# Kernel optimization log

Measured on AMD Instinct MI355X. Metric: run time of the kernel, lower is better.

Reference implementation:

```python
import jax, jax.numpy as jnp
import numpy as np

N_NODES = 32768
N_EDGES = 262144
HEAD = 8
CHANNEL = 64
LAYER_NUM = 2
HC = HEAD * CHANNEL  # 512


def setup_inputs() -> dict:
    key = jax.random.key(0)
    ks = jax.random.split(key, 12)
    def lin(k, fan_in, fan_out):
        s = 1.0 / np.sqrt(fan_in)
        kw, kb = jax.random.split(k)
        W = jax.random.uniform(kw, (fan_in, fan_out), jnp.float32, -s, s)
        b = jax.random.uniform(kb, (fan_out,), jnp.float32, -s, s)
        return W, b
    Wn, bn = lin(ks[0], 118, HC)
    We, be = lin(ks[1], 22, HC)
    Wa, ba = lin(ks[2], 2 * HC, HC)
    attn_w = jax.random.normal(ks[3], (1, HEAD, CHANNEL), jnp.float32) * 0.1
    x = jax.random.normal(ks[4], (N_NODES, 118), jnp.float32)
    edge_feat = jax.random.normal(ks[5], (N_EDGES, 22), jnp.float32)
    src = jax.random.randint(ks[6], (N_EDGES,), 0, N_NODES)
    dst = jax.random.randint(ks[7], (N_EDGES,), 0, N_NODES)
    return {"x": x, "edge_feat": edge_feat, "src": src, "dst": dst,
            "Wn": Wn, "bn": bn, "We": We, "be": be, "Wa": Wa, "ba": ba,
            "attn_w": attn_w}


def reference(x, edge_feat, src, dst, Wn, bn, We, be, Wa, ba, attn_w):
    N = x.shape[0]
    H, C = attn_w.shape[1], attn_w.shape[2]
    h = x @ Wn + bn                      # [N, H*C]
    _eh = edge_feat @ We + be            # computed in original forward, never used
    for _ in range(LAYER_NUM):
        # gather src/dst node states onto edges and score them (GATv2 style)
        e = jnp.concatenate([h[src], h[dst]], axis=-1)            # [E, 2HC]
        e = jax.nn.leaky_relu(e @ Wa + ba, negative_slope=0.01)   # [E, HC]
        score = jnp.sum(e.reshape(-1, H, C) * attn_w, axis=-1)    # [E, H]
        # edge softmax normalized over incoming edges of each dst node
        m = jax.ops.segment_max(score, dst, num_segments=N)       # [N, H]
        ex = jnp.exp(score - m[dst])                              # [E, H]
        denom = jax.ops.segment_sum(ex, dst, num_segments=N)      # [N, H]
        alpha = ex / denom[dst]                                   # [E, H]
        # weighted message passing: u_mul_e then sum over dst
        msg = h[src].reshape(-1, H, C) * alpha[:, :, None]        # [E, H, C]
        h = jax.ops.segment_sum(msg, dst, num_segments=N).reshape(N, H * C)
    return h
```

## Files before the change

kernel.cpp:

```cpp
#include <hip/hip_runtime.h>
#include <hip/hip_bf16.h>
#include <stdint.h>

#define N_NODES 32768
#define N_EDGES 262144

typedef __attribute__((ext_vector_type(8))) short short8;
typedef __attribute__((ext_vector_type(4))) float f32x4;

typedef const __attribute__((address_space(1))) void* gvp;
typedef __attribute__((address_space(3))) void* lvp;

__device__ __forceinline__ float bf2f(ushort u) {
  return __uint_as_float(((uint)u) << 16);
}
__device__ __forceinline__ ushort f2bf(float f) {
  uint x = __float_as_uint(f);
  uint r = (x + 0x7fffu + ((x >> 16) & 1u)) >> 16;
  return (ushort)r;
}
__device__ __forceinline__ float loadf(const void* p, size_t i, int isbf) {
  return isbf ? bf2f(((const ushort*)p)[i]) : ((const float*)p)[i];
}

__global__ void detect_dtype(const uint* __restrict__ xw, int* __restrict__ flag) {
  __shared__ int cnt;
  if (threadIdx.x == 0) cnt = 0;
  __syncthreads();
  int good = 0;
  for (int i = threadIdx.x; i < 1024; i += 256) {
    uint lo = xw[i] & 0xFFFFu;
    uint ef = (lo >> 7) & 0xFFu;
    if (lo == 0u || (ef >= 0x60u && ef <= 0x90u)) good++;
  }
  atomicAdd(&cnt, good);
  __syncthreads();
  if (threadIdx.x == 0) *flag = (cnt >= 614) ? 1 : 0;
}

__global__ void prep_weights(const void* __restrict__ Wa, const void* __restrict__ Wn,
                             const void* __restrict__ ba, const void* __restrict__ bn,
                             const void* __restrict__ aw, const int* __restrict__ flag,
                             ushort* __restrict__ W2T, ushort* __restrict__ WnpT,
                             float* __restrict__ bias2, float* __restrict__ bnf,
                             float* __restrict__ wf) {
  const int fl = *flag;
  const int b = blockIdx.x;
  if (b < 2048) {
    int t = b * 256 + threadIdx.x;
    int n = t >> 9, k = t & 511;
    size_t idx = (n < 512) ? ((size_t)k * 512 + n) : ((size_t)(512 + k) * 512 + (n - 512));
    W2T[t] = f2bf(loadf(Wa, idx, fl));
  } else if (b < 2304) {
    int t = (b - 2048) * 256 + threadIdx.x;
    int n = t >> 7, k = t & 127;
    WnpT[t] = (k < 118) ? f2bf(loadf(Wn, (size_t)k * 512 + n, fl)) : (ushort)0;
  } else {
    int t = (b - 2304) * 256 + threadIdx.x;
    if (t < 1024) bias2[t] = (t < 512) ? loadf(ba, t, fl) : 0.f;
    if (t < 512) { bnf[t] = loadf(bn, t, fl); wf[t] = loadf(aw, t, fl); }
  }
}

__global__ void build_xp(const void* __restrict__ x, const int* __restrict__ flag,
                         ushort* __restrict__ xp) {
  int fl = *flag;
  int t = blockIdx.x * blockDim.x + threadIdx.x;
  int i = t >> 7, k = t & 127;
  xp[t] = (k < 118) ? f2bf(loadf(x, (size_t)i * 118 + k, fl)) : (ushort)0;
}

__global__ void csr_count(const int* __restrict__ dst, int* __restrict__ cnt) {
  int e = blockIdx.x * blockDim.x + threadIdx.x;
  atomicAdd(&cnt[dst[e]], 1);
}

__global__ __launch_bounds__(1024)
void csr_scan(const int* __restrict__ cnt, int* __restrict__ rowptr,
              int* __restrict__ cursor) {
  __shared__ int part[1024];
  const int t = threadIdx.x;
  const int base = t * 32;
  int loc[32];
  int s = 0;
#pragma unroll
  for (int i = 0; i < 32; ++i) { loc[i] = s; s += cnt[base + i]; }
  part[t] = s;
  __syncthreads();
  for (int off = 1; off < 1024; off <<= 1) {
    int v = (t >= off) ? part[t - off] : 0;
    __syncthreads();
    part[t] += v;
    __syncthreads();
  }
  int pre = (t == 0) ? 0 : part[t - 1];
#pragma unroll
  for (int i = 0; i < 32; ++i) {
    int v = pre + loc[i];
    rowptr[base + i] = v;
    cursor[base + i] = v;
  }
  if (t == 1023) rowptr[N_NODES] = part[1023];
}

__global__ void csr_fill(const int* __restrict__ dst, int* __restrict__ cursor,
                         int* __restrict__ eidx) {
  int e = blockIdx.x * blockDim.x + threadIdx.x;
  int p = atomicAdd(&cursor[dst[e]], 1);
  eidx[p] = e;
}

__global__ __launch_bounds__(256)
void gemm_bf16(const ushort* __restrict__ A, const ushort* __restrict__ BT,
               const float* __restrict__ bias, ushort* __restrict__ C,
               int M, int N, int K) {
  __shared__ __align__(16) ushort As[128 * 32];
  __shared__ __align__(16) ushort Bs[128 * 32];
  const int tid = threadIdx.x, wave = tid >> 6, lane = tid & 63;
  const int bm = blockIdx.y * 128, bn = blockIdx.x * 128;
  const int wm = (wave >> 1) * 64, wn = (wave & 1) * 64;
  const int fcol = lane & 15, quad = lane >> 4;

  const f32x4 zero = {0.f, 0.f, 0.f, 0.f};
  f32x4 acc[4][4];
#pragma unroll
  for (int i = 0; i < 4; ++i)
#pragma unroll
    for (int j = 0; j < 4; ++j) acc[i][j] = zero;

  for (int k0 = 0; k0 < K; k0 += 32) {
#pragma unroll
    for (int r = 0; r < 2; ++r) {
      int o = r * 4096 + wave * 1024 + lane * 16;
      int row = o >> 6;
      int ke = (o & 63) >> 1;
      const ushort* gA = A + (size_t)(bm + row) * K + k0 + ke;
      const ushort* gB = BT + (size_t)(bn + row) * K + k0 + ke;
      ushort* lA = As + ((r * 4096 + wave * 1024) >> 1);
      ushort* lB = Bs + ((r * 4096 + wave * 1024) >> 1);
      __builtin_amdgcn_global_load_lds((gvp)(const void*)gA, (lvp)(void*)lA, 16, 0, 0);
      __builtin_amdgcn_global_load_lds((gvp)(const void*)gB, (lvp)(void*)lB, 16, 0, 0);
    }
    __syncthreads();
    short8 a[4], b[4];
#pragma unroll
    for (int i = 0; i < 4; ++i) {
      a[i] = *(const short8*)&As[(wm + i * 16 + fcol) * 32 + quad * 8];
      b[i] = *(const short8*)&Bs[(wn + i * 16 + fcol) * 32 + quad * 8];
    }
#pragma unroll
    for (int i = 0; i < 4; ++i)
#pragma unroll
      for (int j = 0; j < 4; ++j)
        acc[i][j] = __builtin_amdgcn_mfma_f32_16x16x32_bf16(a[i], b[j], acc[i][j], 0, 0, 0);
    __syncthreads();
  }

#pragma unroll
  for (int i = 0; i < 4; ++i) {
    int rowb = bm + wm + i * 16 + quad * 4;
#pragma unroll
    for (int j = 0; j < 4; ++j) {
      int col = bn + wn + j * 16 + fcol;
      float bb = bias[col];
#pragma unroll
      for (int r = 0; r < 4; ++r) {
        C[(size_t)(rowb + r) * N + col] = f2bf(acc[i][j][r] + bb);
      }
    }
  }
}

__global__ __launch_bounds__(256)
void node_fused(const ushort* __restrict__ PQ, const ushort* __restrict__ hb_in,
                const int* __restrict__ src, const int* __restrict__ eidx,
                const int* __restrict__ rowptr, const float* __restrict__ wf,
                const int* __restrict__ flag, ushort* __restrict__ hb_out,
                void* __restrict__ out, int write_out) {
  const int wave = threadIdx.x >> 6, lane = threadIdx.x & 63;
  const int d = blockIdx.x * 4 + wave;
  const int beg = rowptr[d], end = rowptr[d + 1];
  const int c0 = lane * 8;

  const uint4 qv = *(const uint4*)(PQ + (size_t)d * 1024 + 512 + c0);
  const uint qw[4] = {qv.x, qv.y, qv.z, qv.w};
  float q[8], w[8];
#pragma unroll
  for (int i = 0; i < 4; ++i) {
    q[2 * i]     = __uint_as_float(qw[i] << 16);
    q[2 * i + 1] = __uint_as_float(qw[i] & 0xffff0000u);
  }
  const float4 w0 = *(const float4*)(wf + c0);
  const float4 w1 = *(const float4*)(wf + c0 + 4);
  w[0] = w0.x; w[1] = w0.y; w[2] = w0.z; w[3] = w0.w;
  w[4] = w1.x; w[5] = w1.y; w[6] = w1.z; w[7] = w1.w;

  float m = -3e38f, den = 0.f;
  float acc[8] = {0.f, 0.f, 0.f, 0.f, 0.f, 0.f, 0.f, 0.f};

  int sj = (beg < end) ? src[eidx[beg]] : 0;
  for (int j = beg; j < end; ++j) {
    const int s = sj;
    if (j + 1 < end) sj = src[eidx[j + 1]];
    const uint4 pv = *(const uint4*)(PQ + (size_t)s * 1024 + c0);
    const uint4 hv = *(const uint4*)(hb_in + (size_t)s * 512 + c0);
    const uint pw[4] = {pv.x, pv.y, pv.z, pv.w};
    const uint hw[4] = {hv.x, hv.y, hv.z, hv.w};
    float t = 0.f;
#pragma unroll
    for (int i = 0; i < 4; ++i) {
      float ea = __uint_as_float(pw[i] << 16) + q[2 * i];
      float eb = __uint_as_float(pw[i] & 0xffff0000u) + q[2 * i + 1];
      ea = (ea > 0.f) ? ea : 0.01f * ea;
      eb = (eb > 0.f) ? eb : 0.01f * eb;
      t += ea * w[2 * i] + eb * w[2 * i + 1];
    }
    t += __shfl_xor(t, 1);
    t += __shfl_xor(t, 2);
    t += __shfl_xor(t, 4);
    const float mnew = fmaxf(m, t);
    const float corr = __expf(m - mnew);
    const float ex = __expf(t - mnew);
    den = den * corr + ex;
#pragma unroll
    for (int i = 0; i < 4; ++i) {
      acc[2 * i]     = acc[2 * i] * corr     + ex * __uint_as_float(hw[i] << 16);
      acc[2 * i + 1] = acc[2 * i + 1] * corr + ex * __uint_as_float(hw[i] & 0xffff0000u);
    }
    m = mnew;
  }

  const float inv = (end > beg) ? (1.f / den) : 0.f;
  uint o[4];
#pragma unroll
  for (int i = 0; i < 4; ++i) {
    float v0 = acc[2 * i] * inv, v1 = acc[2 * i + 1] * inv;
    o[i] = (uint)f2bf(v0) | ((uint)f2bf(v1) << 16);
  }
  *(uint4*)(hb_out + (size_t)d * 512 + c0) = *(uint4*)o;
  if (write_out) {
    if (*flag) {
      *(uint4*)((ushort*)out + (size_t)d * 512 + c0) = *(uint4*)o;
    } else {
      float4 f0 = {acc[0] * inv, acc[1] * inv, acc[2] * inv, acc[3] * inv};
      float4 f1 = {acc[4] * inv, acc[5] * inv, acc[6] * inv, acc[7] * inv};
      *(float4*)((float*)out + (size_t)d * 512 + c0) = f0;
      *(float4*)((float*)out + (size_t)d * 512 + c0 + 4) = f1;
    }
  }
}

extern "C" void kernel_launch(void* const* d_in, const int* in_sizes, int n_in,
                              void* d_out, int out_size, void* d_ws, size_t ws_size,
                              hipStream_t stream) {
  const void* x   = d_in[0];
  const int*  src = (const int*)d_in[2];
  const int*  dst = (const int*)d_in[3];
  const void* Wn  = d_in[4];
  const void* bn  = d_in[5];
  const void* Wa  = d_in[8];
  const void* ba  = d_in[9];
  const void* aw  = d_in[10];

  char* ws = (char*)d_ws;
  size_t off = 0;
  auto alloc = [&](size_t bytes) {
    char* p = ws + off;
    off = (off + bytes + 255) & ~(size_t)255;
    return p;
  };
  ushort* hbA    = (ushort*)alloc((size_t)N_NODES * 512 * 2);
  ushort* hbB    = (ushort*)alloc((size_t)N_NODES * 512 * 2);
  ushort* PQ     = (ushort*)alloc((size_t)N_NODES * 1024 * 2);
  int*    eidx   = (int*)   alloc((size_t)N_EDGES * 4);
  int*    rowptr = (int*)   alloc((size_t)(N_NODES + 1) * 4);
  int*    cnt    = (int*)   alloc((size_t)N_NODES * 4);
  int*    cursor = (int*)   alloc((size_t)N_NODES * 4);
  ushort* W2T    = (ushort*)alloc((size_t)1024 * 512 * 2);
  float*  bias2  = (float*) alloc(1024 * 4);
  ushort* xp     = (ushort*)alloc((size_t)N_NODES * 128 * 2);
  ushort* WnpT   = (ushort*)alloc((size_t)512 * 128 * 2);
  float*  bnf    = (float*) alloc(512 * 4);
  float*  wf     = (float*) alloc(512 * 4);
  int*    flag   = (int*)   alloc(256);

  detect_dtype<<<1, 256, 0, stream>>>((const uint*)x, flag);
  prep_weights<<<2308, 256, 0, stream>>>(Wa, Wn, ba, bn, aw, flag,
                                         W2T, WnpT, bias2, bnf, wf);
  build_xp<<<(N_NODES * 128) / 256, 256, 0, stream>>>(x, flag, xp);

  hipMemsetAsync(cnt, 0, (size_t)N_NODES * 4, stream);
  csr_count<<<N_EDGES / 256, 256, 0, stream>>>(dst, cnt);
  csr_scan<<<1, 1024, 0, stream>>>(cnt, rowptr, cursor);
  csr_fill<<<N_EDGES / 256, 256, 0, stream>>>(dst, cursor, eidx);

  {
    dim3 g(512 / 128, N_NODES / 128);
    gemm_bf16<<<g, 256, 0, stream>>>(xp, WnpT, bnf, hbA, N_NODES, 512, 128);
  }

  ushort* hin = hbA;
  ushort* hout = hbB;
  for (int layer = 0; layer < 2; ++layer) {
    dim3 g(1024 / 128, N_NODES / 128);
    gemm_bf16<<<g, 256, 0, stream>>>(hin, W2T, bias2, PQ, N_NODES, 1024, 512);
    node_fused<<<N_NODES / 4, 256, 0, stream>>>(PQ, hin, src, eidx, rowptr, wf, flag,
                                                hout, d_out, layer == 1 ? 1 : 0);
    ushort* t = hin; hin = hout; hout = t;
  }
}
```

Baseline: 486.0 us.

## Fold node projection into first-layer attention GEMM and skip redundant softmax rescale

Precomputes a combined weight Wc = Wn·Wa and a bias bc = bn·Wa + ba, so the layer-0 PQ GEMM runs with K=128 on the padded input x instead of K=512 on h. This removes most of the first-layer GEMM work. It also merges build_xp into the weight prep kernel, and in the online softmax it skips the max-correction exps when no lane's score exceeds the running max. The cost is a different rounding path (bf16 of the product weight), a few small extra prep launches, and a wave-uniform branch in the inner loop.

```diff
diff --git a/kernel.cpp b/kernel.cpp
--- a/kernel.cpp
+++ b/kernel.cpp
@@ -38,12 +38,14 @@
   if (threadIdx.x == 0) *flag = (cnt >= 614) ? 1 : 0;
 }
 
-__global__ void prep_weights(const void* __restrict__ Wa, const void* __restrict__ Wn,
-                             const void* __restrict__ ba, const void* __restrict__ bn,
-                             const void* __restrict__ aw, const int* __restrict__ flag,
-                             ushort* __restrict__ W2T, ushort* __restrict__ WnpT,
-                             float* __restrict__ bias2, float* __restrict__ bnf,
-                             float* __restrict__ wf) {
+__global__ void prep_all(const void* __restrict__ Wa, const void* __restrict__ Wn,
+                         const void* __restrict__ ba, const void* __restrict__ bn,
+                         const void* __restrict__ aw, const void* __restrict__ x,
+                         const int* __restrict__ flag,
+                         ushort* __restrict__ W2T, ushort* __restrict__ WnpT,
+                         ushort* __restrict__ Wn_pad, float* __restrict__ bias2,
+                         float* __restrict__ bnf, float* __restrict__ wf,
+                         float* __restrict__ zbias, ushort* __restrict__ xp) {
   const int fl = *flag;
   const int b = blockIdx.x;
   if (b < 2048) {
@@ -55,19 +57,41 @@
     int t = (b - 2048) * 256 + threadIdx.x;
     int n = t >> 7, k = t & 127;
     WnpT[t] = (k < 118) ? f2bf(loadf(Wn, (size_t)k * 512 + n, fl)) : (ushort)0;
-  } else {
+  } else if (b < 2560) {
     int t = (b - 2304) * 256 + threadIdx.x;
+    int n = t >> 9, j = t & 511;
+    Wn_pad[t] = (n < 118) ? f2bf(loadf(Wn, (size_t)n * 512 + j, fl)) : (ushort)0;
+  } else if (b < 2564) {
+    int t = (b - 2560) * 256 + threadIdx.x;
     if (t < 1024) bias2[t] = (t < 512) ? loadf(ba, t, fl) : 0.f;
     if (t < 512) { bnf[t] = loadf(bn, t, fl); wf[t] = loadf(aw, t, fl); }
-  }
-}
-
-__global__ void build_xp(const void* __restrict__ x, const int* __restrict__ flag,
-                         ushort* __restrict__ xp) {
-  int fl = *flag;
-  int t = blockIdx.x * blockDim.x + threadIdx.x;
-  int i = t >> 7, k = t & 127;
-  xp[t] = (k < 118) ? f2bf(loadf(x, (size_t)i * 118 + k, fl)) : (ushort)0;
+    if (t < 128) zbias[t] = 0.f;
+  } else {
+    int t = (b - 2564) * 256 + threadIdx.x;
+    int i = t >> 7, k = t & 127;
+    xp[t] = (k < 118) ? f2bf(loadf(x, (size_t)i * 118 + k, fl)) : (ushort)0;
+  }
+}
+
+__global__ __launch_bounds__(256)
+void build_bc(const ushort* __restrict__ W2T, const float* __restrict__ bnf,
+              const float* __restrict__ bias2, float* __restrict__ bc) {
+  const int wave = threadIdx.x >> 6, lane = threadIdx.x & 63;
+  const int j = blockIdx.x * 4 + wave;
+  const uint4 v = *(const uint4*)(W2T + (size_t)j * 512 + lane * 8);
+  const float4 b0 = *(const float4*)(bnf + lane * 8);
+  const float4 b1 = *(const float4*)(bnf + lane * 8 + 4);
+  const uint w[4] = {v.x, v.y, v.z, v.w};
+  const float bb[8] = {b0.x, b0.y, b0.z, b0.w, b1.x, b1.y, b1.z, b1.w};
+  float s = 0.f;
+#pragma unroll
+  for (int i = 0; i < 4; ++i) {
+    s += __uint_as_float(w[i] << 16) * bb[2 * i];
+    s += __uint_as_float(w[i] & 0xffff0000u) * bb[2 * i + 1];
+  }
+  s += __shfl_xor(s, 1);  s += __shfl_xor(s, 2);  s += __shfl_xor(s, 4);
+  s += __shfl_xor(s, 8);  s += __shfl_xor(s, 16); s += __shfl_xor(s, 32);
+  if (lane == 0) bc[j] = s + bias2[j];
 }
 
 __global__ void csr_count(const int* __restrict__ dst, int* __restrict__ cnt) {
@@ -218,16 +242,26 @@
     t += __shfl_xor(t, 1);
     t += __shfl_xor(t, 2);
     t += __shfl_xor(t, 4);
-    const float mnew = fmaxf(m, t);
-    const float corr = __expf(m - mnew);
-    const float ex = __expf(t - mnew);
-    den = den * corr + ex;
-#pragma unroll
-    for (int i = 0; i < 4; ++i) {
-      acc[2 * i]     = acc[2 * i] * corr     + ex * __uint_as_float(hw[i] << 16);
-      acc[2 * i + 1] = acc[2 * i + 1] * corr + ex * __uint_as_float(hw[i] & 0xffff0000u);
-    }
-    m = mnew;
+    if (__any(t > m)) {
+      const float mnew = fmaxf(m, t);
+      const float corr = __expf(m - mnew);
+      const float ex = __expf(t - mnew);
+      den = den * corr + ex;
+#pragma unroll
+      for (int i = 0; i < 4; ++i) {
+        acc[2 * i]     = acc[2 * i] * corr     + ex * __uint_as_float(hw[i] << 16);
+        acc[2 * i + 1] = acc[2 * i + 1] * corr + ex * __uint_as_float(hw[i] & 0xffff0000u);
+      }
+      m = mnew;
+    } else {
+      const float ex = __expf(t - m);
+      den += ex;
+#pragma unroll
+      for (int i = 0; i < 4; ++i) {
+        acc[2 * i]     += ex * __uint_as_float(hw[i] << 16);
+        acc[2 * i + 1] += ex * __uint_as_float(hw[i] & 0xffff0000u);
+      }
+    }
   }
 
   const float inv = (end > beg) ? (1.f / den) : 0.f;
@@ -277,7 +311,11 @@
   int*    cnt    = (int*)   alloc((size_t)N_NODES * 4);
   int*    cursor = (int*)   alloc((size_t)N_NODES * 4);
   ushort* W2T    = (ushort*)alloc((size_t)1024 * 512 * 2);
+  ushort* WcT    = (ushort*)alloc((size_t)1024 * 128 * 2);
+  ushort* Wn_pad = (ushort*)alloc((size_t)128 * 512 * 2);
   float*  bias2  = (float*) alloc(1024 * 4);
+  float*  bc     = (float*) alloc(1024 * 4);
+  float*  zbias  = (float*) alloc(128 * 4);
   ushort* xp     = (ushort*)alloc((size_t)N_NODES * 128 * 2);
   ushort* WnpT   = (ushort*)alloc((size_t)512 * 128 * 2);
   float*  bnf    = (float*) alloc(512 * 4);
@@ -285,9 +323,13 @@
   int*    flag   = (int*)   alloc(256);
 
   detect_dtype<<<1, 256, 0, stream>>>((const uint*)x, flag);
-  prep_weights<<<2308, 256, 0, stream>>>(Wa, Wn, ba, bn, aw, flag,
-                                         W2T, WnpT, bias2, bnf, wf);
-  build_xp<<<(N_NODES * 128) / 256, 256, 0, stream>>>(x, flag, xp);
+  prep_all<<<2564 + (N_NODES * 128) / 256, 256, 0, stream>>>(
+      Wa, Wn, ba, bn, aw, x, flag, W2T, WnpT, Wn_pad, bias2, bnf, wf, zbias, xp);
+  build_bc<<<256, 256, 0, stream>>>(W2T, bnf, bias2, bc);
+  {
+    dim3 g(128 / 128, 1024 / 128);
+    gemm_bf16<<<g, 256, 0, stream>>>(W2T, Wn_pad, zbias, WcT, 1024, 128, 512);
+  }
 
   hipMemsetAsync(cnt, 0, (size_t)N_NODES * 4, stream);
   csr_count<<<N_EDGES / 256, 256, 0, stream>>>(dst, cnt);
@@ -299,13 +341,17 @@
     gemm_bf16<<<g, 256, 0, stream>>>(xp, WnpT, bnf, hbA, N_NODES, 512, 128);
   }
 
-  ushort* hin = hbA;
-  ushort* hout = hbB;
-  for (int layer = 0; layer < 2; ++layer) {
+  {
     dim3 g(1024 / 128, N_NODES / 128);
-    gemm_bf16<<<g, 256, 0, stream>>>(hin, W2T, bias2, PQ, N_NODES, 1024, 512);
-    node_fused<<<N_NODES / 4, 256, 0, stream>>>(PQ, hin, src, eidx, rowptr, wf, flag,
-                                                hout, d_out, layer == 1 ? 1 : 0);
-    ushort* t = hin; hin = hout; hout = t;
-  }
-}
+    gemm_bf16<<<g, 256, 0, stream>>>(xp, WcT, bc, PQ, N_NODES, 1024, 128);
+  }
+  node_fused<<<N_NODES / 4, 256, 0, stream>>>(PQ, hbA, src, eidx, rowptr, wf, flag,
+                                              hbB, d_out, 0);
+
+  {
+    dim3 g(1024 / 128, N_NODES / 128);
+    gemm_bf16<<<g, 256, 0, stream>>>(hbB, W2T, bias2, PQ, N_NODES, 1024, 512);
+  }
+  node_fused<<<N_NODES / 4, 256, 0, stream>>>(PQ, hbB, src, eidx, rowptr, wf, flag,
+                                              hbA, d_out, 1);
+}
```

New measurement: 460.8 us. -5.2%, faster.
